# Kernel tuning notes

Hardware: AMD Instinct MI355X
Metric: run time of the kernel (lower is better)

Reference implementation:

```python
import math
import jax, jax.numpy as jnp
import numpy as np

D_MODEL = 256
N_HEAD = 8
D_HEAD = D_MODEL // N_HEAD
GROUP = 8  # window side
SCALE = D_HEAD ** (-0.5)


def _window_partition(x):
    # x: [B, N, C] with N = hw*hw, hw divisible by GROUP
    B, N, C = x.shape
    hw = int(math.isqrt(N))
    ng = hw // GROUP                      # windows per side
    gs = GROUP * GROUP                    # tokens per window
    x = x.reshape(B, ng, GROUP, ng, GROUP, C)
    x = x.transpose(0, 1, 3, 2, 4, 5)     # [B, ng, ng, g, g, C]
    x = x.reshape(B, ng * ng, gs, N_HEAD, D_HEAD)
    return x.transpose(0, 1, 3, 2, 4)     # [B, nw, H, gs, d]


def _window_merge(x, B, N, C):
    # x: [B, nw, H, gs, d] -> [B, N, C]
    hw = int(math.isqrt(N))
    ng = hw // GROUP
    gs = GROUP * GROUP
    x = x.transpose(0, 1, 3, 2, 4)        # [B, nw, gs, H, d]
    x = x.reshape(B, ng, ng, GROUP, GROUP, C)
    x = x.transpose(0, 1, 3, 2, 4, 5)     # [B, ng, g, ng, g, C]
    return x.reshape(B, N, C)


def setup_inputs() -> dict:
    key = jax.random.key(0)
    kq, kk, kv, kw = jax.random.split(key, 4)
    B, N, C = 8, 16384, D_MODEL
    q = jax.random.normal(kq, (B, N, C), dtype=jnp.float32)
    k = jax.random.normal(kk, (B, N, C), dtype=jnp.float32)
    v = jax.random.normal(kv, (B, N, C), dtype=jnp.float32)
    W_fc = jax.random.normal(kw, (C, C), dtype=jnp.float32) * 0.02  # nn.Linear weight [out, in]
    return {"q": q, "k": k, "v": v, "W_fc": W_fc}


def reference(q, k, v, W_fc):
    B, N, C = q.shape
    qw = _window_partition(q)   # [B, nw, H, gs, d]
    kw_ = _window_partition(k)
    vw = _window_partition(v)
    attn = jnp.einsum('bwhqd,bwhkd->bwhqk', qw, kw_) * SCALE
    attn = jax.nn.softmax(attn, axis=-1)
    out = jnp.einsum('bwhqk,bwhkd->bwhqd', attn, vw)
    out = _window_merge(out, B, N, C)      # [B, N, C]
    return out @ W_fc.T
```

## Files before the change

### kernel.cpp

```cpp
#include <hip/hip_runtime.h>
#include <hip/hip_bf16.h>


typedef __attribute__((ext_vector_type(8))) short bf8;
typedef __attribute__((ext_vector_type(4))) float f4;

#define SCALE 0.17677669529663687f
#define CC (SCALE * 1.4426950408889634f)

static __device__ __forceinline__ unsigned short f2bf(float x) {
  unsigned u = __float_as_uint(x);
  u += 0x7FFFu + ((u >> 16) & 1u);
  return (unsigned short)(u >> 16);
}
static __device__ __forceinline__ unsigned pk2(float a, float b) {
  return (unsigned)f2bf(a) | ((unsigned)f2bf(b) << 16);
}
union FragU { unsigned u[4]; bf8 v; };

static __device__ __forceinline__ bf8 load_bf8_f32(const float* __restrict__ p) {
  float4 a = *(const float4*)p;
  float4 b = *(const float4*)(p + 4);
  FragU f;
  f.u[0] = pk2(a.x, a.y);
  f.u[1] = pk2(a.z, a.w);
  f.u[2] = pk2(b.x, b.y);
  f.u[3] = pk2(b.z, b.w);
  return f.v;
}

__global__ void wcvt(const float* __restrict__ W, unsigned short* __restrict__ Wb) {
  const int i = (blockIdx.x * 256 + threadIdx.x) * 4;
  float4 w = *(const float4*)(W + i);
  ushort4 o;
  o.x = f2bf(w.x); o.y = f2bf(w.y); o.z = f2bf(w.z); o.w = f2bf(w.w);
  *(ushort4*)(Wb + i) = o;
}

template <bool WB16>
__global__ __launch_bounds__(256, 4) void win_attn_fc(
    const float* __restrict__ q, const float* __restrict__ k,
    const float* __restrict__ v, const void* __restrict__ Wp,
    float* __restrict__ out) {
  __shared__ unsigned short smem[16896];
  const int tid  = threadIdx.x;
  const int wave = tid >> 6;
  const int lane = tid & 63;
  const int g    = lane >> 4;
  const int c16  = lane & 15;

  const int blk = blockIdx.x;
  const int b   = blk >> 8;
  const int wy  = (blk >> 4) & 15;
  const int wx  = blk & 15;
  const long tokbase = (long)b * 16384 + (long)(wy * 8) * 128 + wx * 8;

  unsigned short* VT = smem + wave * 2304;

  unsigned opk[2][2][4][2];

  const int  srcA = c16 + ((g & 1) << 5);
  const bool hi   = (g >> 1) != 0;

  #pragma unroll
  for (int hh = 0; hh < 2; ++hh) {
    const int h = wave * 2 + hh;

    {
      const long vr = tokbase + (lane >> 3) * 128 + (lane & 7);
      const float* vp = v + vr * 256 + h * 32;
      #pragma unroll
      for (int j = 0; j < 8; ++j) {
        float4 vv = *(const float4*)(vp + 4 * j);
        VT[(4*j+0)*72 + lane] = f2bf(vv.x);
        VT[(4*j+1)*72 + lane] = f2bf(vv.y);
        VT[(4*j+2)*72 + lane] = f2bf(vv.z);
        VT[(4*j+3)*72 + lane] = f2bf(vv.w);
      }
    }

    bf8 qf[4], kf[4];
    #pragma unroll
    for (int t = 0; t < 4; ++t) {
      const int m = 16 * t + c16;
      const long r = tokbase + (m >> 3) * 128 + (m & 7);
      qf[t] = load_bf8_f32(q + r * 256 + h * 32 + g * 8);
      kf[t] = load_bf8_f32(k + r * 256 + h * 32 + g * 8);
    }

    #pragma unroll
    for (int ti = 0; ti < 4; ++ti) {
      f4 st[4];
      #pragma unroll
      for (int tj = 0; tj < 4; ++tj) {
        f4 z = {0.f, 0.f, 0.f, 0.f};
        st[tj] = __builtin_amdgcn_mfma_f32_16x16x32_bf16(kf[tj], qf[ti], z, 0, 0, 0);
      }
      float mx = st[0][0];
      #pragma unroll
      for (int tj = 0; tj < 4; ++tj)
        #pragma unroll
        for (int r = 0; r < 4; ++r) mx = fmaxf(mx, st[tj][r]);
      mx = fmaxf(mx, __shfl_xor(mx, 16));
      mx = fmaxf(mx, __shfl_xor(mx, 32));
      const float mm = mx * CC;
      float pe[4][4];
      float ds = 0.f;
      #pragma unroll
      for (int tj = 0; tj < 4; ++tj)
        #pragma unroll
        for (int r = 0; r < 4; ++r) {
          float p = exp2f(st[tj][r] * CC - mm);
          pe[tj][r] = p;
          ds += p;
        }
      ds += __shfl_xor(ds, 16);
      ds += __shfl_xor(ds, 32);
      const float rc = 1.0f / ds;
      unsigned PW[4][2];
      #pragma unroll
      for (int tj = 0; tj < 4; ++tj) {
        PW[tj][0] = pk2(pe[tj][0] * rc, pe[tj][1] * rc);
        PW[tj][1] = pk2(pe[tj][2] * rc, pe[tj][3] * rc);
      }
      f4 acc0 = {0.f, 0.f, 0.f, 0.f};
      f4 acc1 = {0.f, 0.f, 0.f, 0.f};
      #pragma unroll
      for (int kt = 0; kt < 2; ++kt) {
        unsigned a0 = __shfl(PW[2*kt  ][0], srcA);
        unsigned a1 = __shfl(PW[2*kt  ][1], srcA);
        unsigned a2 = __shfl(PW[2*kt  ][0], srcA + 16);
        unsigned a3 = __shfl(PW[2*kt  ][1], srcA + 16);
        unsigned b0 = __shfl(PW[2*kt+1][0], srcA);
        unsigned b1 = __shfl(PW[2*kt+1][1], srcA);
        unsigned b2 = __shfl(PW[2*kt+1][0], srcA + 16);
        unsigned b3 = __shfl(PW[2*kt+1][1], srcA + 16);
        FragU pf;
        pf.u[0] = hi ? b0 : a0;
        pf.u[1] = hi ? b1 : a1;
        pf.u[2] = hi ? b2 : a2;
        pf.u[3] = hi ? b3 : a3;
        bf8 vf0 = *(const bf8*)(VT + (c16     ) * 72 + 32*kt + 8*g);
        bf8 vf1 = *(const bf8*)(VT + (16 + c16) * 72 + 32*kt + 8*g);
        acc0 = __builtin_amdgcn_mfma_f32_16x16x32_bf16(vf0, pf.v, acc0, 0, 0, 0);
        acc1 = __builtin_amdgcn_mfma_f32_16x16x32_bf16(vf1, pf.v, acc1, 0, 0, 0);
      }
      opk[hh][0][ti][0] = pk2(acc0[0], acc0[1]);
      opk[hh][0][ti][1] = pk2(acc0[2], acc0[3]);
      opk[hh][1][ti][0] = pk2(acc1[0], acc1[1]);
      opk[hh][1][ti][1] = pk2(acc1[2], acc1[3]);
    }
  }

  __syncthreads();
  unsigned short* inter = smem;
  #pragma unroll
  for (int hh = 0; hh < 2; ++hh)
    #pragma unroll
    for (int dt = 0; dt < 2; ++dt)
      #pragma unroll
      for (int ti = 0; ti < 4; ++ti) {
        const int addr = (16*ti + c16) * 264 + (wave*2 + hh) * 32 + 16*dt + 4*g;
        uint2 wv;
        wv.x = opk[hh][dt][ti][0];
        wv.y = opk[hh][dt][ti][1];
        *(uint2*)(inter + addr) = wv;
      }
  __syncthreads();

  f4 acc[4][4];
  #pragma unroll
  for (int mt = 0; mt < 4; ++mt)
    #pragma unroll
    for (int nt = 0; nt < 4; ++nt) {
      f4 z = {0.f, 0.f, 0.f, 0.f};
      acc[mt][nt] = z;
    }
  const float* Wf          = (const float*)Wp;
  const unsigned short* Wb = (const unsigned short*)Wp;
  #pragma unroll
  for (int ks = 0; ks < 8; ++ks) {
    bf8 af[4], wf[4];
    #pragma unroll
    for (int mt = 0; mt < 4; ++mt)
      af[mt] = *(const bf8*)(inter + (16*mt + c16) * 264 + 32*ks + 8*g);
    #pragma unroll
    for (int nt = 0; nt < 4; ++nt) {
      const long widx = (long)(64*wave + 16*nt + c16) * 256 + 32*ks + 8*g;
      if (WB16) wf[nt] = *(const bf8*)(Wb + widx);
      else      wf[nt] = load_bf8_f32(Wf + widx);
    }
    #pragma unroll
    for (int mt = 0; mt < 4; ++mt)
      #pragma unroll
      for (int nt = 0; nt < 4; ++nt)
        acc[mt][nt] = __builtin_amdgcn_mfma_f32_16x16x32_bf16(af[mt], wf[nt], acc[mt][nt], 0, 0, 0);
  }

  #pragma unroll
  for (int mt = 0; mt < 4; ++mt) {
    #pragma unroll
    for (int r = 0; r < 4; ++r) {
      const int m = 16*mt + 4*g + r;
      const long row = tokbase + (m >> 3) * 128 + (m & 7);
      float* op = out + row * 256 + 64*wave + c16;
      #pragma unroll
      for (int nt = 0; nt < 4; ++nt)
        op[16*nt] = acc[mt][nt][r];
    }
  }
}

extern "C" void kernel_launch(void* const* d_in, const int* in_sizes, int n_in,
                              void* d_out, int out_size, void* d_ws, size_t ws_size,
                              hipStream_t stream) {
  const float* q = (const float*)d_in[0];
  const float* k = (const float*)d_in[1];
  const float* v = (const float*)d_in[2];
  const float* W = (const float*)d_in[3];
  float* out = (float*)d_out;
  const int B = in_sizes[0] / (16384 * 256);
  const size_t wbytes = 65536 * sizeof(unsigned short);
  if (ws_size >= wbytes) {
    wcvt<<<dim3(64), dim3(256), 0, stream>>>(W, (unsigned short*)d_ws);
    win_attn_fc<true><<<dim3(B * 256), dim3(256), 0, stream>>>(q, k, v, d_ws, out);
  } else {
    win_attn_fc<false><<<dim3(B * 256), dim3(256), 0, stream>>>(q, k, v, W, out);
  }
}
```

Measured before the change: 134.3 us.

## Use one wave per head with 512-thread blocks, swizzled V transpose, deferred normalization

Result: slower. 164.3 us (+22.4%).

```diff
diff --git a/kernel.cpp b/kernel.cpp
--- a/kernel.cpp
+++ b/kernel.cpp
@@ -38,16 +38,17 @@
 }
 
 template <bool WB16>
-__global__ __launch_bounds__(256, 4) void win_attn_fc(
+__global__ __launch_bounds__(512, 8) void win_attn_fc(
     const float* __restrict__ q, const float* __restrict__ k,
     const float* __restrict__ v, const void* __restrict__ Wp,
     float* __restrict__ out) {
-  __shared__ unsigned short smem[16896];
+  __shared__ unsigned short smem[18432];
   const int tid  = threadIdx.x;
   const int wave = tid >> 6;
   const int lane = tid & 63;
   const int g    = lane >> 4;
   const int c16  = lane & 15;
+  const int h    = wave;
 
   const int blk = blockIdx.x;
   const int b   = blk >> 8;
@@ -57,122 +58,116 @@
 
   unsigned short* VT = smem + wave * 2304;
 
-  unsigned opk[2][2][4][2];
+  unsigned opk[2][4][2];
 
   const int  srcA = c16 + ((g & 1) << 5);
   const bool hi   = (g >> 1) != 0;
 
-  #pragma unroll
-  for (int hh = 0; hh < 2; ++hh) {
-    const int h = wave * 2 + hh;
-
-    {
-      const long vr = tokbase + (lane >> 3) * 128 + (lane & 7);
-      const float* vp = v + vr * 256 + h * 32;
+  const int v_tcol = lane >> 3;
+  const int v_cg   = lane & 7;
+
+  bf8 qf[4], kf[4];
+  #pragma unroll
+  for (int t = 0; t < 4; ++t) {
+    const int m = 16 * t + c16;
+    const long r = tokbase + (m >> 3) * 128 + (m & 7);
+    qf[t] = load_bf8_f32(q + r * 256 + h * 32 + g * 8);
+    kf[t] = load_bf8_f32(k + r * 256 + h * 32 + g * 8);
+  }
+
+  #pragma unroll
+  for (int i = 0; i < 8; ++i) {
+    const long r = tokbase + i * 128 + v_tcol;
+    float4 vv = *(const float4*)(v + r * 256 + h * 32 + v_cg * 4);
+    const int tswz = 8 * (i ^ v_cg) + v_tcol;
+    VT[(4*v_cg + 0) * 72 + tswz] = f2bf(vv.x);
+    VT[(4*v_cg + 1) * 72 + tswz] = f2bf(vv.y);
+    VT[(4*v_cg + 2) * 72 + tswz] = f2bf(vv.z);
+    VT[(4*v_cg + 3) * 72 + tswz] = f2bf(vv.w);
+  }
+
+  #pragma unroll
+  for (int ti = 0; ti < 4; ++ti) {
+    f4 st[4];
+    __builtin_amdgcn_s_setprio(1);
+    #pragma unroll
+    for (int tj = 0; tj < 4; ++tj) {
+      f4 z = {0.f, 0.f, 0.f, 0.f};
+      st[tj] = __builtin_amdgcn_mfma_f32_16x16x32_bf16(kf[tj], qf[ti], z, 0, 0, 0);
+    }
+    __builtin_amdgcn_s_setprio(0);
+    float mx = st[0][0];
+    #pragma unroll
+    for (int tj = 0; tj < 4; ++tj)
       #pragma unroll
-      for (int j = 0; j < 8; ++j) {
-        float4 vv = *(const float4*)(vp + 4 * j);
-        VT[(4*j+0)*72 + lane] = f2bf(vv.x);
-        VT[(4*j+1)*72 + lane] = f2bf(vv.y);
-        VT[(4*j+2)*72 + lane] = f2bf(vv.z);
-        VT[(4*j+3)*72 + lane] = f2bf(vv.w);
-      }
-    }
-
-    bf8 qf[4], kf[4];
-    #pragma unroll
-    for (int t = 0; t < 4; ++t) {
-      const int m = 16 * t + c16;
-      const long r = tokbase + (m >> 3) * 128 + (m & 7);
-      qf[t] = load_bf8_f32(q + r * 256 + h * 32 + g * 8);
-      kf[t] = load_bf8_f32(k + r * 256 + h * 32 + g * 8);
-    }
-
-    #pragma unroll
-    for (int ti = 0; ti < 4; ++ti) {
-      f4 st[4];
-      #pragma unroll
-      for (int tj = 0; tj < 4; ++tj) {
-        f4 z = {0.f, 0.f, 0.f, 0.f};
-        st[tj] = __builtin_amdgcn_mfma_f32_16x16x32_bf16(kf[tj], qf[ti], z, 0, 0, 0);
-      }
-      float mx = st[0][0];
-      #pragma unroll
-      for (int tj = 0; tj < 4; ++tj)
-        #pragma unroll
-        for (int r = 0; r < 4; ++r) mx = fmaxf(mx, st[tj][r]);
-      mx = fmaxf(mx, __shfl_xor(mx, 16));
-      mx = fmaxf(mx, __shfl_xor(mx, 32));
-      const float mm = mx * CC;
-      float pe[4][4];
-      float ds = 0.f;
-      #pragma unroll
-      for (int tj = 0; tj < 4; ++tj)
-        #pragma unroll
-        for (int r = 0; r < 4; ++r) {
-          float p = exp2f(st[tj][r] * CC - mm);
-          pe[tj][r] = p;
-          ds += p;
-        }
-      ds += __shfl_xor(ds, 16);
-      ds += __shfl_xor(ds, 32);
-      const float rc = 1.0f / ds;
-      unsigned PW[4][2];
-      #pragma unroll
-      for (int tj = 0; tj < 4; ++tj) {
-        PW[tj][0] = pk2(pe[tj][0] * rc, pe[tj][1] * rc);
-        PW[tj][1] = pk2(pe[tj][2] * rc, pe[tj][3] * rc);
-      }
-      f4 acc0 = {0.f, 0.f, 0.f, 0.f};
-      f4 acc1 = {0.f, 0.f, 0.f, 0.f};
-      #pragma unroll
-      for (int kt = 0; kt < 2; ++kt) {
-        unsigned a0 = __shfl(PW[2*kt  ][0], srcA);
-        unsigned a1 = __shfl(PW[2*kt  ][1], srcA);
-        unsigned a2 = __shfl(PW[2*kt  ][0], srcA + 16);
-        unsigned a3 = __shfl(PW[2*kt  ][1], srcA + 16);
-        unsigned b0 = __shfl(PW[2*kt+1][0], srcA);
-        unsigned b1 = __shfl(PW[2*kt+1][1], srcA);
-        unsigned b2 = __shfl(PW[2*kt+1][0], srcA + 16);
-        unsigned b3 = __shfl(PW[2*kt+1][1], srcA + 16);
-        FragU pf;
-        pf.u[0] = hi ? b0 : a0;
-        pf.u[1] = hi ? b1 : a1;
-        pf.u[2] = hi ? b2 : a2;
-        pf.u[3] = hi ? b3 : a3;
-        bf8 vf0 = *(const bf8*)(VT + (c16     ) * 72 + 32*kt + 8*g);
-        bf8 vf1 = *(const bf8*)(VT + (16 + c16) * 72 + 32*kt + 8*g);
-        acc0 = __builtin_amdgcn_mfma_f32_16x16x32_bf16(vf0, pf.v, acc0, 0, 0, 0);
-        acc1 = __builtin_amdgcn_mfma_f32_16x16x32_bf16(vf1, pf.v, acc1, 0, 0, 0);
-      }
-      opk[hh][0][ti][0] = pk2(acc0[0], acc0[1]);
-      opk[hh][0][ti][1] = pk2(acc0[2], acc0[3]);
-      opk[hh][1][ti][0] = pk2(acc1[0], acc1[1]);
-      opk[hh][1][ti][1] = pk2(acc1[2], acc1[3]);
-    }
+      for (int r = 0; r < 4; ++r) mx = fmaxf(mx, st[tj][r]);
+    mx = fmaxf(mx, __shfl_xor(mx, 16));
+    mx = fmaxf(mx, __shfl_xor(mx, 32));
+    const float mm = mx * CC;
+    float ds = 0.f;
+    unsigned PW[4][2];
+    #pragma unroll
+    for (int tj = 0; tj < 4; ++tj) {
+      float p0 = exp2f(st[tj][0] * CC - mm);
+      float p1 = exp2f(st[tj][1] * CC - mm);
+      float p2 = exp2f(st[tj][2] * CC - mm);
+      float p3 = exp2f(st[tj][3] * CC - mm);
+      ds += (p0 + p1) + (p2 + p3);
+      PW[tj][0] = pk2(p0, p1);
+      PW[tj][1] = pk2(p2, p3);
+    }
+    ds += __shfl_xor(ds, 16);
+    ds += __shfl_xor(ds, 32);
+    const float rc = 1.0f / ds;
+    f4 acc0 = {0.f, 0.f, 0.f, 0.f};
+    f4 acc1 = {0.f, 0.f, 0.f, 0.f};
+    #pragma unroll
+    for (int kt = 0; kt < 2; ++kt) {
+      unsigned a0 = __shfl(PW[2*kt  ][0], srcA);
+      unsigned a1 = __shfl(PW[2*kt  ][1], srcA);
+      unsigned a2 = __shfl(PW[2*kt  ][0], srcA + 16);
+      unsigned a3 = __shfl(PW[2*kt  ][1], srcA + 16);
+      unsigned b0 = __shfl(PW[2*kt+1][0], srcA);
+      unsigned b1 = __shfl(PW[2*kt+1][1], srcA);
+      unsigned b2 = __shfl(PW[2*kt+1][0], srcA + 16);
+      unsigned b3 = __shfl(PW[2*kt+1][1], srcA + 16);
+      FragU pf;
+      pf.u[0] = hi ? b0 : a0;
+      pf.u[1] = hi ? b1 : a1;
+      pf.u[2] = hi ? b2 : a2;
+      pf.u[3] = hi ? b3 : a3;
+      bf8 vf0 = *(const bf8*)(VT + (c16     ) * 72 + 8 * ((4*kt + g) ^ (c16 >> 2)));
+      bf8 vf1 = *(const bf8*)(VT + (16 + c16) * 72 + 8 * ((4*kt + g) ^ (4 + (c16 >> 2))));
+      __builtin_amdgcn_s_setprio(1);
+      acc0 = __builtin_amdgcn_mfma_f32_16x16x32_bf16(vf0, pf.v, acc0, 0, 0, 0);
+      acc1 = __builtin_amdgcn_mfma_f32_16x16x32_bf16(vf1, pf.v, acc1, 0, 0, 0);
+      __builtin_amdgcn_s_setprio(0);
+    }
+    opk[0][ti][0] = pk2(acc0[0] * rc, acc0[1] * rc);
+    opk[0][ti][1] = pk2(acc0[2] * rc, acc0[3] * rc);
+    opk[1][ti][0] = pk2(acc1[0] * rc, acc1[1] * rc);
+    opk[1][ti][1] = pk2(acc1[2] * rc, acc1[3] * rc);
   }
 
   __syncthreads();
   unsigned short* inter = smem;
   #pragma unroll
-  for (int hh = 0; hh < 2; ++hh)
-    #pragma unroll
-    for (int dt = 0; dt < 2; ++dt)
-      #pragma unroll
-      for (int ti = 0; ti < 4; ++ti) {
-        const int addr = (16*ti + c16) * 264 + (wave*2 + hh) * 32 + 16*dt + 4*g;
-        uint2 wv;
-        wv.x = opk[hh][dt][ti][0];
-        wv.y = opk[hh][dt][ti][1];
-        *(uint2*)(inter + addr) = wv;
-      }
+  for (int dt = 0; dt < 2; ++dt)
+    #pragma unroll
+    for (int ti = 0; ti < 4; ++ti) {
+      const int addr = (16*ti + c16) * 264 + h * 32 + 16*dt + 4*g;
+      uint2 wv;
+      wv.x = opk[dt][ti][0];
+      wv.y = opk[dt][ti][1];
+      *(uint2*)(inter + addr) = wv;
+    }
   __syncthreads();
 
-  f4 acc[4][4];
+  f4 acc[4][2];
   #pragma unroll
   for (int mt = 0; mt < 4; ++mt)
     #pragma unroll
-    for (int nt = 0; nt < 4; ++nt) {
+    for (int nt = 0; nt < 2; ++nt) {
       f4 z = {0.f, 0.f, 0.f, 0.f};
       acc[mt][nt] = z;
     }
@@ -180,21 +175,23 @@
   const unsigned short* Wb = (const unsigned short*)Wp;
   #pragma unroll
   for (int ks = 0; ks < 8; ++ks) {
-    bf8 af[4], wf[4];
+    bf8 af[4], wf[2];
     #pragma unroll
     for (int mt = 0; mt < 4; ++mt)
       af[mt] = *(const bf8*)(inter + (16*mt + c16) * 264 + 32*ks + 8*g);
     #pragma unroll
-    for (int nt = 0; nt < 4; ++nt) {
-      const long widx = (long)(64*wave + 16*nt + c16) * 256 + 32*ks + 8*g;
+    for (int nt = 0; nt < 2; ++nt) {
+      const long widx = (long)(32*wave + 16*nt + c16) * 256 + 32*ks + 8*g;
       if (WB16) wf[nt] = *(const bf8*)(Wb + widx);
       else      wf[nt] = load_bf8_f32(Wf + widx);
     }
+    __builtin_amdgcn_s_setprio(1);
     #pragma unroll
     for (int mt = 0; mt < 4; ++mt)
       #pragma unroll
-      for (int nt = 0; nt < 4; ++nt)
+      for (int nt = 0; nt < 2; ++nt)
         acc[mt][nt] = __builtin_amdgcn_mfma_f32_16x16x32_bf16(af[mt], wf[nt], acc[mt][nt], 0, 0, 0);
+    __builtin_amdgcn_s_setprio(0);
   }
 
   #pragma unroll
@@ -203,9 +200,9 @@
     for (int r = 0; r < 4; ++r) {
       const int m = 16*mt + 4*g + r;
       const long row = tokbase + (m >> 3) * 128 + (m & 7);
-      float* op = out + row * 256 + 64*wave + c16;
+      float* op = out + row * 256 + 32*wave + c16;
       #pragma unroll
-      for (int nt = 0; nt < 4; ++nt)
+      for (int nt = 0; nt < 2; ++nt)
         op[16*nt] = acc[mt][nt][r];
     }
   }
@@ -223,8 +220,8 @@
   const size_t wbytes = 65536 * sizeof(unsigned short);
   if (ws_size >= wbytes) {
     wcvt<<<dim3(64), dim3(256), 0, stream>>>(W, (unsigned short*)d_ws);
-    win_attn_fc<true><<<dim3(B * 256), dim3(256), 0, stream>>>(q, k, v, d_ws, out);
+    win_attn_fc<true><<<dim3(B * 256), dim3(512), 0, stream>>>(q, k, v, d_ws, out);
   } else {
-    win_attn_fc<false><<<dim3(B * 256), dim3(256), 0, stream>>>(q, k, v, W, out);
-  }
-}
+    win_attn_fc<false><<<dim3(B * 256), dim3(512), 0, stream>>>(q, k, v, W, out);
+  }
+}
```

## Split fused window attention and FC projection into separate kernels via bf16 workspace

Applied to the files above, without the earlier changes.

Result: slower. 188.3 us (+40.2%).

```diff
diff --git a/kernel.cpp b/kernel.cpp
--- a/kernel.cpp
+++ b/kernel.cpp
@@ -35,6 +35,199 @@
   ushort4 o;
   o.x = f2bf(w.x); o.y = f2bf(w.y); o.z = f2bf(w.z); o.w = f2bf(w.w);
   *(ushort4*)(Wb + i) = o;
+}
+
+__global__ __launch_bounds__(512, 7) void win_attn(
+    const float* __restrict__ q, const float* __restrict__ k,
+    const float* __restrict__ v, unsigned short* __restrict__ attnout) {
+  __shared__ unsigned short smem[18432];
+  const int tid  = threadIdx.x;
+  const int wave = tid >> 6;
+  const int lane = tid & 63;
+  const int g    = lane >> 4;
+  const int c16  = lane & 15;
+  const int h    = wave;
+
+  const int blk = blockIdx.x;
+  const int b   = blk >> 8;
+  const int wy  = (blk >> 4) & 15;
+  const int wx  = blk & 15;
+  const long tokbase = (long)b * 16384 + (long)(wy * 8) * 128 + wx * 8;
+
+  unsigned short* VT = smem + wave * 2304;
+
+  const int  srcA = c16 + ((g & 1) << 5);
+  const bool hi   = (g >> 1) != 0;
+  const int v_tcol = lane >> 3;
+  const int v_cg   = lane & 7;
+
+  #pragma unroll
+  for (int i = 0; i < 8; ++i) {
+    const long r = tokbase + i * 128 + v_tcol;
+    float4 vv = *(const float4*)(v + r * 256 + h * 32 + v_cg * 4);
+    const int tswz = 8 * (i ^ v_cg) + v_tcol;
+    VT[(4*v_cg + 0) * 72 + tswz] = f2bf(vv.x);
+    VT[(4*v_cg + 1) * 72 + tswz] = f2bf(vv.y);
+    VT[(4*v_cg + 2) * 72 + tswz] = f2bf(vv.z);
+    VT[(4*v_cg + 3) * 72 + tswz] = f2bf(vv.w);
+  }
+
+  bf8 kf[4];
+  #pragma unroll
+  for (int t = 0; t < 4; ++t) {
+    const int m = 16 * t + c16;
+    const long r = tokbase + (m >> 3) * 128 + (m & 7);
+    kf[t] = load_bf8_f32(k + r * 256 + h * 32 + g * 8);
+  }
+
+  unsigned opk[2][4][2];
+
+  #pragma unroll
+  for (int ti = 0; ti < 4; ++ti) {
+    const int m = 16 * ti + c16;
+    const long rq = tokbase + (m >> 3) * 128 + (m & 7);
+    bf8 qfi = load_bf8_f32(q + rq * 256 + h * 32 + g * 8);
+
+    f4 st[4];
+    __builtin_amdgcn_s_setprio(1);
+    #pragma unroll
+    for (int tj = 0; tj < 4; ++tj) {
+      f4 z = {0.f, 0.f, 0.f, 0.f};
+      st[tj] = __builtin_amdgcn_mfma_f32_16x16x32_bf16(kf[tj], qfi, z, 0, 0, 0);
+    }
+    __builtin_amdgcn_s_setprio(0);
+
+    float mx = st[0][0];
+    #pragma unroll
+    for (int tj = 0; tj < 4; ++tj)
+      #pragma unroll
+      for (int r = 0; r < 4; ++r) mx = fmaxf(mx, st[tj][r]);
+    mx = fmaxf(mx, __shfl_xor(mx, 16));
+    mx = fmaxf(mx, __shfl_xor(mx, 32));
+    const float mm = mx * CC;
+
+    float ds = 0.f;
+    unsigned PW[4][2];
+    #pragma unroll
+    for (int tj = 0; tj < 4; ++tj) {
+      float p0 = exp2f(st[tj][0] * CC - mm);
+      float p1 = exp2f(st[tj][1] * CC - mm);
+      float p2 = exp2f(st[tj][2] * CC - mm);
+      float p3 = exp2f(st[tj][3] * CC - mm);
+      ds += (p0 + p1) + (p2 + p3);
+      PW[tj][0] = pk2(p0, p1);
+      PW[tj][1] = pk2(p2, p3);
+    }
+    ds += __shfl_xor(ds, 16);
+    ds += __shfl_xor(ds, 32);
+    const float rc = 1.0f / ds;
+
+    f4 acc0 = {0.f, 0.f, 0.f, 0.f};
+    f4 acc1 = {0.f, 0.f, 0.f, 0.f};
+    #pragma unroll
+    for (int kt = 0; kt < 2; ++kt) {
+      unsigned a0 = __shfl(PW[2*kt  ][0], srcA);
+      unsigned a1 = __shfl(PW[2*kt  ][1], srcA);
+      unsigned a2 = __shfl(PW[2*kt  ][0], srcA + 16);
+      unsigned a3 = __shfl(PW[2*kt  ][1], srcA + 16);
+      unsigned b0 = __shfl(PW[2*kt+1][0], srcA);
+      unsigned b1 = __shfl(PW[2*kt+1][1], srcA);
+      unsigned b2 = __shfl(PW[2*kt+1][0], srcA + 16);
+      unsigned b3 = __shfl(PW[2*kt+1][1], srcA + 16);
+      FragU pf;
+      pf.u[0] = hi ? b0 : a0;
+      pf.u[1] = hi ? b1 : a1;
+      pf.u[2] = hi ? b2 : a2;
+      pf.u[3] = hi ? b3 : a3;
+      bf8 vf0 = *(const bf8*)(VT + (c16     ) * 72 + 8 * ((4*kt + g) ^ (c16 >> 2)));
+      bf8 vf1 = *(const bf8*)(VT + (16 + c16) * 72 + 8 * ((4*kt + g) ^ (4 + (c16 >> 2))));
+      __builtin_amdgcn_s_setprio(1);
+      acc0 = __builtin_amdgcn_mfma_f32_16x16x32_bf16(vf0, pf.v, acc0, 0, 0, 0);
+      acc1 = __builtin_amdgcn_mfma_f32_16x16x32_bf16(vf1, pf.v, acc1, 0, 0, 0);
+      __builtin_amdgcn_s_setprio(0);
+    }
+    opk[0][ti][0] = pk2(acc0[0] * rc, acc0[1] * rc);
+    opk[0][ti][1] = pk2(acc0[2] * rc, acc0[3] * rc);
+    opk[1][ti][0] = pk2(acc1[0] * rc, acc1[1] * rc);
+    opk[1][ti][1] = pk2(acc1[2] * rc, acc1[3] * rc);
+  }
+
+  #pragma unroll
+  for (int dt = 0; dt < 2; ++dt)
+    #pragma unroll
+    for (int ti = 0; ti < 4; ++ti) {
+      const int T = 16*ti + c16;
+      uint2 wv;
+      wv.x = opk[dt][ti][0];
+      wv.y = opk[dt][ti][1];
+      *(uint2*)(VT + T * 36 + 16*dt + 4*g) = wv;
+    }
+
+  {
+    const int t = lane;
+    const long row = tokbase + (t >> 3) * 128 + (t & 7);
+    const unsigned short* src = VT + t * 36;
+    unsigned short* dst = attnout + row * 256 + h * 32;
+    #pragma unroll
+    for (int c = 0; c < 4; ++c) {
+      uint2 aa = *(const uint2*)(src + 8*c);
+      uint2 bb = *(const uint2*)(src + 8*c + 4);
+      uint4 o;
+      o.x = aa.x; o.y = aa.y; o.z = bb.x; o.w = bb.y;
+      *(uint4*)(dst + 8*c) = o;
+    }
+  }
+}
+
+__global__ __launch_bounds__(256, 4) void fc_gemm(
+    const unsigned short* __restrict__ A,
+    const unsigned short* __restrict__ Wb,
+    float* __restrict__ out) {
+  const int tid  = threadIdx.x;
+  const int wave = tid >> 6;
+  const int lane = tid & 63;
+  const int g    = lane >> 4;
+  const int c16  = lane & 15;
+  const long mbase = (long)blockIdx.x * 64;
+
+  f4 acc[4][4];
+  #pragma unroll
+  for (int mt = 0; mt < 4; ++mt)
+    #pragma unroll
+    for (int nt = 0; nt < 4; ++nt) {
+      f4 z = {0.f, 0.f, 0.f, 0.f};
+      acc[mt][nt] = z;
+    }
+
+  #pragma unroll
+  for (int ks = 0; ks < 8; ++ks) {
+    bf8 af[4], wf[4];
+    #pragma unroll
+    for (int mt = 0; mt < 4; ++mt)
+      af[mt] = *(const bf8*)(A + (mbase + 16*mt + c16) * 256 + 32*ks + 8*g);
+    #pragma unroll
+    for (int nt = 0; nt < 4; ++nt)
+      wf[nt] = *(const bf8*)(Wb + (long)(64*wave + 16*nt + c16) * 256 + 32*ks + 8*g);
+    __builtin_amdgcn_s_setprio(1);
+    #pragma unroll
+    for (int mt = 0; mt < 4; ++mt)
+      #pragma unroll
+      for (int nt = 0; nt < 4; ++nt)
+        acc[mt][nt] = __builtin_amdgcn_mfma_f32_16x16x32_bf16(af[mt], wf[nt], acc[mt][nt], 0, 0, 0);
+    __builtin_amdgcn_s_setprio(0);
+  }
+
+  #pragma unroll
+  for (int mt = 0; mt < 4; ++mt) {
+    #pragma unroll
+    for (int r = 0; r < 4; ++r) {
+      const long row = mbase + 16*mt + 4*g + r;
+      float* op = out + row * 256 + 64*wave + c16;
+      #pragma unroll
+      for (int nt = 0; nt < 4; ++nt)
+        op[16*nt] = acc[mt][nt][r];
+    }
+  }
 }
 
 template <bool WB16>
@@ -48,24 +241,18 @@
   const int lane = tid & 63;
   const int g    = lane >> 4;
   const int c16  = lane & 15;
-
   const int blk = blockIdx.x;
   const int b   = blk >> 8;
   const int wy  = (blk >> 4) & 15;
   const int wx  = blk & 15;
   const long tokbase = (long)b * 16384 + (long)(wy * 8) * 128 + wx * 8;
-
   unsigned short* VT = smem + wave * 2304;
-
   unsigned opk[2][2][4][2];
-
   const int  srcA = c16 + ((g & 1) << 5);
   const bool hi   = (g >> 1) != 0;
-
   #pragma unroll
   for (int hh = 0; hh < 2; ++hh) {
     const int h = wave * 2 + hh;
-
     {
       const long vr = tokbase + (lane >> 3) * 128 + (lane & 7);
       const float* vp = v + vr * 256 + h * 32;
@@ -78,7 +265,6 @@
         VT[(4*j+3)*72 + lane] = f2bf(vv.w);
       }
     }
-
     bf8 qf[4], kf[4];
     #pragma unroll
     for (int t = 0; t < 4; ++t) {
@@ -87,7 +273,6 @@
       qf[t] = load_bf8_f32(q + r * 256 + h * 32 + g * 8);
       kf[t] = load_bf8_f32(k + r * 256 + h * 32 + g * 8);
     }
-
     #pragma unroll
     for (int ti = 0; ti < 4; ++ti) {
       f4 st[4];
@@ -104,25 +289,21 @@
       mx = fmaxf(mx, __shfl_xor(mx, 16));
       mx = fmaxf(mx, __shfl_xor(mx, 32));
       const float mm = mx * CC;
-      float pe[4][4];
       float ds = 0.f;
-      #pragma unroll
-      for (int tj = 0; tj < 4; ++tj)
-        #pragma unroll
-        for (int r = 0; r < 4; ++r) {
-          float p = exp2f(st[tj][r] * CC - mm);
-          pe[tj][r] = p;
-          ds += p;
-        }
+      unsigned PW[4][2];
+      #pragma unroll
+      for (int tj = 0; tj < 4; ++tj) {
+        float p0 = exp2f(st[tj][0] * CC - mm);
+        float p1 = exp2f(st[tj][1] * CC - mm);
+        float p2 = exp2f(st[tj][2] * CC - mm);
+        float p3 = exp2f(st[tj][3] * CC - mm);
+        ds += (p0 + p1) + (p2 + p3);
+        PW[tj][0] = pk2(p0, p1);
+        PW[tj][1] = pk2(p2, p3);
+      }
       ds += __shfl_xor(ds, 16);
       ds += __shfl_xor(ds, 32);
       const float rc = 1.0f / ds;
-      unsigned PW[4][2];
-      #pragma unroll
-      for (int tj = 0; tj < 4; ++tj) {
-        PW[tj][0] = pk2(pe[tj][0] * rc, pe[tj][1] * rc);
-        PW[tj][1] = pk2(pe[tj][2] * rc, pe[tj][3] * rc);
-      }
       f4 acc0 = {0.f, 0.f, 0.f, 0.f};
       f4 acc1 = {0.f, 0.f, 0.f, 0.f};
       #pragma unroll
@@ -145,13 +326,12 @@
         acc0 = __builtin_amdgcn_mfma_f32_16x16x32_bf16(vf0, pf.v, acc0, 0, 0, 0);
         acc1 = __builtin_amdgcn_mfma_f32_16x16x32_bf16(vf1, pf.v, acc1, 0, 0, 0);
       }
-      opk[hh][0][ti][0] = pk2(acc0[0], acc0[1]);
-      opk[hh][0][ti][1] = pk2(acc0[2], acc0[3]);
-      opk[hh][1][ti][0] = pk2(acc1[0], acc1[1]);
-      opk[hh][1][ti][1] = pk2(acc1[2], acc1[3]);
-    }
-  }
-
+      opk[hh][0][ti][0] = pk2(acc0[0] * rc, acc0[1] * rc);
+      opk[hh][0][ti][1] = pk2(acc0[2] * rc, acc0[3] * rc);
+      opk[hh][1][ti][0] = pk2(acc1[0] * rc, acc1[1] * rc);
+      opk[hh][1][ti][1] = pk2(acc1[2] * rc, acc1[3] * rc);
+    }
+  }
   __syncthreads();
   unsigned short* inter = smem;
   #pragma unroll
@@ -167,7 +347,6 @@
         *(uint2*)(inter + addr) = wv;
       }
   __syncthreads();
-
   f4 acc[4][4];
   #pragma unroll
   for (int mt = 0; mt < 4; ++mt)
@@ -196,7 +375,6 @@
       for (int nt = 0; nt < 4; ++nt)
         acc[mt][nt] = __builtin_amdgcn_mfma_f32_16x16x32_bf16(af[mt], wf[nt], acc[mt][nt], 0, 0, 0);
   }
-
   #pragma unroll
   for (int mt = 0; mt < 4; ++mt) {
     #pragma unroll
@@ -220,8 +398,19 @@
   const float* W = (const float*)d_in[3];
   float* out = (float*)d_out;
   const int B = in_sizes[0] / (16384 * 256);
-  const size_t wbytes = 65536 * sizeof(unsigned short);
-  if (ws_size >= wbytes) {
+  const long M = (long)B * 16384;
+
+  const size_t wbytes  = 65536 * sizeof(unsigned short);
+  const size_t abytes  = (size_t)M * 256 * sizeof(unsigned short);
+  const size_t need    = wbytes + abytes;
+
+  if (ws_size >= need) {
+    unsigned short* Wb = (unsigned short*)d_ws;
+    unsigned short* Ab = (unsigned short*)((char*)d_ws + wbytes);
+    wcvt<<<dim3(64), dim3(256), 0, stream>>>(W, Wb);
+    win_attn<<<dim3(B * 256), dim3(512), 0, stream>>>(q, k, v, Ab);
+    fc_gemm<<<dim3((int)(M / 64)), dim3(256), 0, stream>>>(Ab, Wb, out);
+  } else if (ws_size >= wbytes) {
     wcvt<<<dim3(64), dim3(256), 0, stream>>>(W, (unsigned short*)d_ws);
     win_attn_fc<true><<<dim3(B * 256), dim3(256), 0, stream>>>(q, k, v, d_ws, out);
   } else {
```
